# Kernel tuning notes

Measured on AMD Instinct MI355X. Metric: run time of the kernel, lower is better.

The kernel has to match this reference:

```python
import jax, jax.numpy as jnp
import numpy as np

BATCH = 16384
IN_DIM = 256
UNITS = 256


def setup_inputs() -> dict:
    key = jax.random.key(0)
    ks = jax.random.split(key, 5)
    scale = 1.0 / np.sqrt(IN_DIM + UNITS)
    return {
        "x": jax.random.normal(ks[0], (BATCH, IN_DIM), dtype=jnp.float32),
        "prev_h": jax.random.normal(ks[1], (BATCH, UNITS), dtype=jnp.float32),
        "Wz": jax.random.normal(ks[2], (IN_DIM + UNITS, UNITS), dtype=jnp.float32) * scale,
        "bz": jnp.zeros((UNITS,), dtype=jnp.float32),
        "Wr": jax.random.normal(ks[3], (IN_DIM + UNITS, UNITS), dtype=jnp.float32) * scale,
        "br": jnp.zeros((UNITS,), dtype=jnp.float32),
        "Ws": jax.random.normal(ks[4], (IN_DIM + UNITS, UNITS), dtype=jnp.float32) * scale,
        "bs": jnp.zeros((UNITS,), dtype=jnp.float32),
    }


def reference(x, prev_h, Wz, bz, Wr, br, Ws, bs):
    # concat order matches the TF module: [prev_h, x]
    concat = jnp.concatenate([prev_h, x], axis=1)  # [B, units+in_dim]
    z = jax.nn.sigmoid(concat @ Wz + bz)
    r = jax.nn.sigmoid(concat @ Wr + br)
    concat_cand = jnp.concatenate([r * prev_h, x], axis=1)
    h_tilda = jnp.tanh(concat_cand @ Ws + bs)
    h_new = (1.0 - z) * prev_h + z * h_tilda
    return h_new
```

## Files before the change

kernel.cpp:

```cpp
#include <hip/hip_runtime.h>
#include <hip/hip_bf16.h>


#define BATCH 16384
#define UNITS 256
#define KDIM 512
#define ROWS 64

typedef float f32x4 __attribute__((ext_vector_type(4)));
typedef __bf16 bf16x8 __attribute__((ext_vector_type(8)));
typedef unsigned short us8 __attribute__((ext_vector_type(8)));
typedef unsigned short us4v __attribute__((ext_vector_type(4)));

static __device__ __forceinline__ unsigned short f2bf(float f) {
    union { float f; unsigned u; } v; v.f = f;
    unsigned r = v.u + 0x7fffu + ((v.u >> 16) & 1u);
    return (unsigned short)(r >> 16);
}
static __device__ __forceinline__ float bf2f(unsigned short u) {
    union { unsigned u; float f; } v; v.u = ((unsigned)u) << 16;
    return v.f;
}

__global__ void pack_weights(const float* __restrict__ Wz,
                             const float* __restrict__ Wr,
                             const float* __restrict__ Ws,
                             unsigned short* __restrict__ out) {
    int gid = blockIdx.x * blockDim.x + threadIdx.x;
    int w   = gid >> 17;
    int rem = gid & 131071;
    int k = rem >> 8;
    int n = rem & 255;
    const float* W = (w == 0) ? Wz : (w == 1) ? Wr : Ws;
    float f = W[rem];
    int kt = k >> 5, kr = k & 31;
    int hi = kr >> 3, j = kr & 7;
    int nt = n >> 4,  lo = n & 15;
    int l  = hi * 16 + lo;
    out[(size_t)w * 131072 + (size_t)(((kt * 16 + nt) * 64 + l) * 8 + j)] = f2bf(f);
}

__launch_bounds__(1024, 4)
__global__ void gru_main(const float* __restrict__ x,
                         const float* __restrict__ ph,
                         const float* __restrict__ bz,
                         const float* __restrict__ br,
                         const float* __restrict__ bs,
                         const unsigned short* __restrict__ Wp,
                         float* __restrict__ out) {
    __shared__ unsigned short sm[ROWS * 512];

    const int tid  = threadIdx.x;
    const int lane = tid & 63;
    const int wid  = tid >> 6;
    const int brow = blockIdx.x * ROWS;

    for (int i = tid; i < 4096; i += 1024) {
        int row = i >> 6;
        int c4  = (i & 63) << 2;
        int swr = (row & 7) << 3;
        float4 a = *(const float4*)&ph[(size_t)(brow + row) * 256 + c4];
        us4v u; u.x = f2bf(a.x); u.y = f2bf(a.y); u.z = f2bf(a.z); u.w = f2bf(a.w);
        *(us4v*)&sm[row * 512 + (c4 ^ swr)] = u;
        float4 b = *(const float4*)&x[(size_t)(brow + row) * 256 + c4];
        us4v v; v.x = f2bf(b.x); v.y = f2bf(b.y); v.z = f2bf(b.z); v.w = f2bf(b.w);
        *(us4v*)&sm[row * 512 + ((256 + c4) ^ swr)] = v;
    }
    __syncthreads();

    const unsigned short* Wz_p = Wp;
    const unsigned short* Wr_p = Wp + 131072;
    const unsigned short* Ws_p = Wp + 262144;

    const int l15 = lane & 15;
    const int kg  = (lane >> 4) << 3;

    f32x4 accz[4] = {};
    f32x4 accr[4] = {};
    for (int kt = 0; kt < 16; ++kt) {
        int ak = kt * 32 + kg;
        size_t bidx = (size_t)(((kt * 16 + wid) * 64 + lane) * 8);
        bf16x8 b0 = __builtin_bit_cast(bf16x8, *(const us8*)(Wz_p + bidx));
        bf16x8 b1 = __builtin_bit_cast(bf16x8, *(const us8*)(Wr_p + bidx));
#pragma unroll
        for (int m = 0; m < 4; ++m) {
            int arow = m * 16 + l15;
            bf16x8 a = __builtin_bit_cast(bf16x8,
                *(const us8*)&sm[arow * 512 + (ak ^ ((arow & 7) << 3))]);
            accz[m] = __builtin_amdgcn_mfma_f32_16x16x32_bf16(a, b0, accz[m], 0, 0, 0);
            accr[m] = __builtin_amdgcn_mfma_f32_16x16x32_bf16(a, b1, accr[m], 0, 0, 0);
        }
    }
    __syncthreads();

    float pst[4][4];
    const int rrow0 = (lane >> 4) * 4;
    const int col   = wid * 16 + l15;
    {
        float bzc = bz[col], brc = br[col];
#pragma unroll
        for (int m = 0; m < 4; ++m) {
#pragma unroll
            for (int i = 0; i < 4; ++i) {
                int lrow = m * 16 + rrow0 + i;
                int addr = lrow * 512 + (col ^ ((lrow & 7) << 3));
                float p = bf2f(sm[addr]);
                float z = 1.f / (1.f + __expf(-(accz[m][i] + bzc)));
                float r = 1.f / (1.f + __expf(-(accr[m][i] + brc)));
                accz[m][i] = z;
                pst[m][i]  = p;
                sm[addr] = f2bf(r * p);
            }
        }
    }
    __syncthreads();

    f32x4 accs[4] = {};
    for (int kt = 0; kt < 16; ++kt) {
        int ak = kt * 32 + kg;
        size_t bidx = (size_t)(((kt * 16 + wid) * 64 + lane) * 8);
        bf16x8 b = __builtin_bit_cast(bf16x8, *(const us8*)(Ws_p + bidx));
#pragma unroll
        for (int m = 0; m < 4; ++m) {
            int arow = m * 16 + l15;
            bf16x8 a = __builtin_bit_cast(bf16x8,
                *(const us8*)&sm[arow * 512 + (ak ^ ((arow & 7) << 3))]);
            accs[m] = __builtin_amdgcn_mfma_f32_16x16x32_bf16(a, b, accs[m], 0, 0, 0);
        }
    }

    {
        float bsc = bs[col];
#pragma unroll
        for (int m = 0; m < 4; ++m) {
#pragma unroll
            for (int i = 0; i < 4; ++i) {
                float s = accs[m][i] + bsc;
                float e = __expf(-2.f * fabsf(s));
                float th = (1.f - e) / (1.f + e);
                th = (s < 0.f) ? -th : th;
                float z = accz[m][i];
                float p = pst[m][i];
                int grow = brow + m * 16 + rrow0 + i;
                out[(size_t)grow * 256 + col] = (1.f - z) * p + z * th;
            }
        }
    }
}

extern "C" void kernel_launch(void* const* d_in, const int* in_sizes, int n_in,
                              void* d_out, int out_size, void* d_ws, size_t ws_size,
                              hipStream_t stream) {
    const float* x  = (const float*)d_in[0];
    const float* ph = (const float*)d_in[1];
    const float* Wz = (const float*)d_in[2];
    const float* bz = (const float*)d_in[3];
    const float* Wr = (const float*)d_in[4];
    const float* br = (const float*)d_in[5];
    const float* Ws = (const float*)d_in[6];
    const float* bs = (const float*)d_in[7];
    unsigned short* Wp = (unsigned short*)d_ws;

    hipLaunchKernelGGL(pack_weights, dim3(1536), dim3(256), 0, stream, Wz, Wr, Ws, Wp);
    hipLaunchKernelGGL(gru_main, dim3(256), dim3(1024), 0, stream,
                       x, ph, bz, br, bs, Wp, (float*)d_out);
}
```

Before: 37.23 us.

## Prefetch weight fragments and write r*h to separate LDS buffer

Register-prefetches the next k-step's packed weight fragments in both GEMM phases so global loads overlap the MFMAs, and issues the first candidate-weight loads before the gate epilogue. The r*prev_h values now go into a separate LDS array instead of overwriting the prev_h region, which removes one __syncthreads between the first GEMM and the gate epilogue. Bias loads move to kernel start. LDS use grows by 32 KB per block (96 KB total), which may limit blocks per CU, and the prefetch registers add register pressure.

```diff
diff --git a/kernel.cpp b/kernel.cpp
--- a/kernel.cpp
+++ b/kernel.cpp
@@ -49,11 +49,26 @@
                          const unsigned short* __restrict__ Wp,
                          float* __restrict__ out) {
     __shared__ unsigned short sm[ROWS * 512];
+    __shared__ unsigned short rh[ROWS * 256];
 
     const int tid  = threadIdx.x;
     const int lane = tid & 63;
     const int wid  = tid >> 6;
     const int brow = blockIdx.x * ROWS;
+
+    const int l15 = lane & 15;
+    const int kg  = (lane >> 4) << 3;
+    const int col = wid * 16 + l15;
+
+    const unsigned short* Wz_p = Wp;
+    const unsigned short* Wr_p = Wp + 131072;
+    const unsigned short* Ws_p = Wp + 262144;
+    const unsigned short* pz = Wz_p + (size_t)((wid * 64 + lane) * 8);
+    const unsigned short* pr = Wr_p + (size_t)((wid * 64 + lane) * 8);
+    const unsigned short* ps = Ws_p + (size_t)((wid * 64 + lane) * 8);
+    us8 b0n = *(const us8*)pz;
+    us8 b1n = *(const us8*)pr;
+    float bzc = bz[col], brc = br[col], bsc = bs[col];
 
     for (int i = tid; i < 4096; i += 1024) {
         int row = i >> 6;
@@ -68,82 +83,90 @@
     }
     __syncthreads();
 
-    const unsigned short* Wz_p = Wp;
-    const unsigned short* Wr_p = Wp + 131072;
-    const unsigned short* Ws_p = Wp + 262144;
-
-    const int l15 = lane & 15;
-    const int kg  = (lane >> 4) << 3;
-
     f32x4 accz[4] = {};
     f32x4 accr[4] = {};
+#pragma unroll 4
     for (int kt = 0; kt < 16; ++kt) {
+        bf16x8 B0 = __builtin_bit_cast(bf16x8, b0n);
+        bf16x8 B1 = __builtin_bit_cast(bf16x8, b1n);
+        if (kt < 15) {
+            b0n = *(const us8*)(pz + (size_t)(kt + 1) * 8192);
+            b1n = *(const us8*)(pr + (size_t)(kt + 1) * 8192);
+        }
         int ak = kt * 32 + kg;
-        size_t bidx = (size_t)(((kt * 16 + wid) * 64 + lane) * 8);
-        bf16x8 b0 = __builtin_bit_cast(bf16x8, *(const us8*)(Wz_p + bidx));
-        bf16x8 b1 = __builtin_bit_cast(bf16x8, *(const us8*)(Wr_p + bidx));
 #pragma unroll
         for (int m = 0; m < 4; ++m) {
             int arow = m * 16 + l15;
             bf16x8 a = __builtin_bit_cast(bf16x8,
                 *(const us8*)&sm[arow * 512 + (ak ^ ((arow & 7) << 3))]);
-            accz[m] = __builtin_amdgcn_mfma_f32_16x16x32_bf16(a, b0, accz[m], 0, 0, 0);
-            accr[m] = __builtin_amdgcn_mfma_f32_16x16x32_bf16(a, b1, accr[m], 0, 0, 0);
+            accz[m] = __builtin_amdgcn_mfma_f32_16x16x32_bf16(a, B0, accz[m], 0, 0, 0);
+            accr[m] = __builtin_amdgcn_mfma_f32_16x16x32_bf16(a, B1, accr[m], 0, 0, 0);
         }
     }
-    __syncthreads();
+
+    us8 s0n = *(const us8*)ps;
+    us8 s1n = *(const us8*)(ps + 8192);
 
     float pst[4][4];
     const int rrow0 = (lane >> 4) * 4;
-    const int col   = wid * 16 + l15;
-    {
-        float bzc = bz[col], brc = br[col];
 #pragma unroll
-        for (int m = 0; m < 4; ++m) {
+    for (int m = 0; m < 4; ++m) {
 #pragma unroll
-            for (int i = 0; i < 4; ++i) {
-                int lrow = m * 16 + rrow0 + i;
-                int addr = lrow * 512 + (col ^ ((lrow & 7) << 3));
-                float p = bf2f(sm[addr]);
-                float z = 1.f / (1.f + __expf(-(accz[m][i] + bzc)));
-                float r = 1.f / (1.f + __expf(-(accr[m][i] + brc)));
-                accz[m][i] = z;
-                pst[m][i]  = p;
-                sm[addr] = f2bf(r * p);
-            }
+        for (int i = 0; i < 4; ++i) {
+            int lrow = m * 16 + rrow0 + i;
+            int cs = col ^ ((lrow & 7) << 3);
+            float p = bf2f(sm[lrow * 512 + cs]);
+            float z = 1.f / (1.f + __expf(-(accz[m][i] + bzc)));
+            float r = 1.f / (1.f + __expf(-(accr[m][i] + brc)));
+            accz[m][i] = z;
+            pst[m][i]  = p;
+            rh[lrow * 256 + cs] = f2bf(r * p);
         }
     }
     __syncthreads();
 
     f32x4 accs[4] = {};
-    for (int kt = 0; kt < 16; ++kt) {
+#pragma unroll 4
+    for (int kt = 0; kt < 8; ++kt) {
+        bf16x8 B = __builtin_bit_cast(bf16x8, s0n);
+        s0n = s1n;
+        s1n = *(const us8*)(ps + (size_t)(kt + 2) * 8192);
         int ak = kt * 32 + kg;
-        size_t bidx = (size_t)(((kt * 16 + wid) * 64 + lane) * 8);
-        bf16x8 b = __builtin_bit_cast(bf16x8, *(const us8*)(Ws_p + bidx));
+#pragma unroll
+        for (int m = 0; m < 4; ++m) {
+            int arow = m * 16 + l15;
+            bf16x8 a = __builtin_bit_cast(bf16x8,
+                *(const us8*)&rh[arow * 256 + (ak ^ ((arow & 7) << 3))]);
+            accs[m] = __builtin_amdgcn_mfma_f32_16x16x32_bf16(a, B, accs[m], 0, 0, 0);
+        }
+    }
+#pragma unroll 4
+    for (int kt = 8; kt < 16; ++kt) {
+        bf16x8 B = __builtin_bit_cast(bf16x8, s0n);
+        s0n = s1n;
+        if (kt < 14) s1n = *(const us8*)(ps + (size_t)(kt + 2) * 8192);
+        int ak = kt * 32 + kg;
 #pragma unroll
         for (int m = 0; m < 4; ++m) {
             int arow = m * 16 + l15;
             bf16x8 a = __builtin_bit_cast(bf16x8,
                 *(const us8*)&sm[arow * 512 + (ak ^ ((arow & 7) << 3))]);
-            accs[m] = __builtin_amdgcn_mfma_f32_16x16x32_bf16(a, b, accs[m], 0, 0, 0);
+            accs[m] = __builtin_amdgcn_mfma_f32_16x16x32_bf16(a, B, accs[m], 0, 0, 0);
         }
     }
 
-    {
-        float bsc = bs[col];
 #pragma unroll
-        for (int m = 0; m < 4; ++m) {
+    for (int m = 0; m < 4; ++m) {
 #pragma unroll
-            for (int i = 0; i < 4; ++i) {
-                float s = accs[m][i] + bsc;
-                float e = __expf(-2.f * fabsf(s));
-                float th = (1.f - e) / (1.f + e);
-                th = (s < 0.f) ? -th : th;
-                float z = accz[m][i];
-                float p = pst[m][i];
-                int grow = brow + m * 16 + rrow0 + i;
-                out[(size_t)grow * 256 + col] = (1.f - z) * p + z * th;
-            }
+        for (int i = 0; i < 4; ++i) {
+            float s = accs[m][i] + bsc;
+            float e = __expf(-2.f * fabsf(s));
+            float th = (1.f - e) / (1.f + e);
+            th = (s < 0.f) ? -th : th;
+            float z = accz[m][i];
+            float p = pst[m][i];
+            int grow = brow + m * 16 + rrow0 + i;
+            out[(size_t)grow * 256 + col] = (1.f - z) * p + z * th;
         }
     }
 }
```

Measured after the change: 34.11 us. 1.09x faster.
